# Kernel optimization log

Measured on AMD Instinct MI355X. Metric: run time of the kernel, lower is better.

## Reference

```python
import jax, jax.numpy as jnp
import numpy as np

B, S, H = 8, 2048, 1024
G, K = 16, 320          # n_groups, codebook_size
D = H // G              # codebook_dim per group


def setup_inputs() -> dict:
    key = jax.random.key(0)
    k1, k2, k3, k4 = jax.random.split(key, 4)
    inputs = jax.random.normal(k1, (B, S, H), jnp.float32)
    attention_mask = jax.random.uniform(k2, (B, S)) < 0.9
    W_cb = jax.random.normal(k3, (D, K), jnp.float32) * 0.05  # shared codebook projection
    b_cb = jnp.zeros((K,), jnp.float32)
    codevectors = jax.random.normal(k4, (K, D), jnp.float32) * 0.05
    return {"inputs": inputs, "attention_mask": attention_mask,
            "W_cb": W_cb, "b_cb": b_cb, "codevectors": codevectors}


def reference(inputs, attention_mask, W_cb, b_cb, codevectors):
    # inputs: [B,S,H]; split H into G groups of D (tensor_split, dim=-1)
    Bs, Ss, Hs = inputs.shape
    Ks, Ds = codevectors.shape
    Gs = Hs // Ds
    x = inputs.reshape(Bs, Ss, Gs, Ds)                              # [B,S,G,D]
    logits = jnp.einsum('bsgd,dk->bsgk', x, W_cb) + b_cb            # grouped codebook logits
    # training path, gumbel_softmax=False: probs = log_softmax(logits).exp() = softmax
    probs = jax.nn.softmax(logits, axis=-1)                         # [B,S,G,K]
    cv = jnp.einsum('bsgk,kd->bsgd', probs, codevectors)            # choice(probs, codevectors)
    cv = cv.reshape(Bs, Ss, Hs)
    # scatter back into zero-padded tensors: positions outside the mask stay zero
    cv = jnp.where(attention_mask[:, :, None], cv, 0.0)             # [B,S,H]
    codewords = jnp.argmax(logits, axis=-1)                         # [B,S,G]
    codewords = jnp.where(attention_mask[:, :, None], codewords, 0)
    return cv, codewords
```

## Files before the change

### kernel.cpp

```cpp
#include <hip/hip_runtime.h>
#include <math.h>

typedef _Float16 f16;
typedef _Float16 f16x2 __attribute__((ext_vector_type(2)));
typedef _Float16 f16x8 __attribute__((ext_vector_type(8)));
typedef short short8 __attribute__((ext_vector_type(8)));
typedef float f32x4 __attribute__((ext_vector_type(4)));

#define NROWS (8 * 2048 * 16)
#define BLOCK 512
#define WAVES 8
#define NITER 8
#define GRID 256
#define TAU2 4.4e-4f
#define LOG2E 1.4426950408889634f
#define MEXP 6.0f
#define EXP2F(x) __builtin_amdgcn_exp2f(x)

__device__ __forceinline__ short f2bf(float f) {
    unsigned u = __builtin_bit_cast(unsigned, f);
    return (short)((u + 0x7fffu + ((u >> 16) & 1u)) >> 16);
}
__device__ __forceinline__ float bf2f(short h) {
    return __builtin_bit_cast(float, ((unsigned)(unsigned short)h) << 16);
}
__device__ __forceinline__ f16x2 pkrtz(float a, float b) {
    return __builtin_bit_cast(f16x2, __builtin_amdgcn_cvt_pkrtz(a, b));
}

template <int HB>
__device__ __forceinline__ void half_pass(
    const short* __restrict__ Wh, const short* __restrict__ Wl,
    const f16* __restrict__ CVp, const float* __restrict__ bs,
    const short8 (&xh)[2], const short8 (&xl)[2],
    int l15, int lg, int wb0, int wb1, int bsb, int cvb,
    f32x4 (&cv)[4], float& sum_run,
    float& m1o, float& m2o, int& i1o, int& c0, int& c1, int& c2)
{
    f32x4 acc[10];
    __builtin_amdgcn_s_setprio(1);
    #pragma unroll
    for (int nt = 0; nt < 10; ++nt) {
        const int ntg = HB / 16 + nt;
        acc[nt] = *(const f32x4*)&bs[ntg * 16 + bsb];
        short8 whf0 = *(const short8*)&Wh[ntg * 1024 + wb0];
        short8 wlf0 = *(const short8*)&Wl[ntg * 1024 + wb0];
        acc[nt] = __builtin_amdgcn_mfma_f32_16x16x32_bf16(whf0, xl[0], acc[nt], 0, 0, 0);
        acc[nt] = __builtin_amdgcn_mfma_f32_16x16x32_bf16(wlf0, xh[0], acc[nt], 0, 0, 0);
        acc[nt] = __builtin_amdgcn_mfma_f32_16x16x32_bf16(whf0, xh[0], acc[nt], 0, 0, 0);
        short8 whf1 = *(const short8*)&Wh[ntg * 1024 + wb1];
        short8 wlf1 = *(const short8*)&Wl[ntg * 1024 + wb1];
        acc[nt] = __builtin_amdgcn_mfma_f32_16x16x32_bf16(whf1, xl[1], acc[nt], 0, 0, 0);
        acc[nt] = __builtin_amdgcn_mfma_f32_16x16x32_bf16(wlf1, xh[1], acc[nt], 0, 0, 0);
        acc[nt] = __builtin_amdgcn_mfma_f32_16x16x32_bf16(whf1, xh[1], acc[nt], 0, 0, 0);
    }
    __builtin_amdgcn_s_setprio(0);

    float m1a = -INFINITY, m2a = -INFINITY, m1b = -INFINITY, m2b = -INFINITY;
    int i1a = HB, i1b = HB + 80;
    #pragma unroll
    for (int nt = 0; nt < 5; ++nt) {
        #pragma unroll
        for (int r = 0; r < 4; ++r) {
            float va = acc[nt][r];
            m2a = fmaxf(m2a, fminf(m1a, va));
            if (va > m1a) { m1a = va; i1a = HB + nt * 16 + lg * 4 + r; }
            float vb = acc[nt + 5][r];
            m2b = fmaxf(m2b, fminf(m1b, vb));
            if (vb > m1b) { m1b = vb; i1b = HB + (nt + 5) * 16 + lg * 4 + r; }
        }
    }

    float sA = 0.f, sB = 0.f, sC = 0.f, sD = 0.f;
    #pragma unroll
    for (int lp = 0; lp < 5; ++lp) {
        const int pg = HB / 32 + lp;
        float q0 = EXP2F(acc[lp * 2][0] - MEXP);
        float q1 = EXP2F(acc[lp * 2][1] - MEXP);
        float q2 = EXP2F(acc[lp * 2][2] - MEXP);
        float q3 = EXP2F(acc[lp * 2][3] - MEXP);
        float q4 = EXP2F(acc[lp * 2 + 1][0] - MEXP);
        float q5 = EXP2F(acc[lp * 2 + 1][1] - MEXP);
        float q6 = EXP2F(acc[lp * 2 + 1][2] - MEXP);
        float q7 = EXP2F(acc[lp * 2 + 1][3] - MEXP);
        sA += q0 + q4; sB += q1 + q5; sC += q2 + q6; sD += q3 + q7;
        f16x2 a01 = pkrtz(q0, q1), a23 = pkrtz(q2, q3);
        f16x2 a45 = pkrtz(q4, q5), a67 = pkrtz(q6, q7);
        f16x8 pf = {a01[0], a01[1], a23[0], a23[1],
                    a45[0], a45[1], a67[0], a67[1]};
        #pragma unroll
        for (int dt = 0; dt < 4; ++dt) {
            f16x8 cf = *(const f16x8*)&CVp[(pg * 4 + dt) * 512 + cvb];
            cv[dt] = __builtin_amdgcn_mfma_f32_16x16x32_f16(cf, pf, cv[dt], 0, 0, 0);
        }
    }
    sum_run += (sA + sB) + (sC + sD);

    float m2 = fmaxf(fmaxf(m2a, m2b), fminf(m1a, m1b));
    float m1 = m1a;
    int i1 = i1a;
    if (m1b > m1) { m1 = m1b; i1 = i1b; }
    #pragma unroll
    for (int dx = 16; dx <= 32; dx <<= 1) {
        float mo = __shfl_xor(m1, dx, 64);
        int io = __shfl_xor(i1, dx, 64);
        float m2x = __shfl_xor(m2, dx, 64);
        m2 = fmaxf(fmaxf(m2, m2x), fminf(m1, mo));
        if (mo > m1 || (mo == m1 && io < i1)) { m1 = mo; i1 = io; }
    }

    c0 = -1; c1 = -1; c2 = -1;
    if (m1 - m2 < TAU2) {
        const float thr = m1 - TAU2;
        #pragma unroll
        for (int nt = 0; nt < 10; ++nt) {
            #pragma unroll
            for (int r = 0; r < 4; ++r) {
                if (acc[nt][r] >= thr) {
                    int c = HB + nt * 16 + lg * 4 + r;
                    if (c0 < 0) c0 = c;
                    else if (c1 < 0) c1 = c;
                    else if (c2 < 0) c2 = c;
                }
            }
        }
    }
    m1o = m1; m2o = m2; i1o = i1;
}

__global__ __launch_bounds__(BLOCK) void vq_mfma(
    const float* __restrict__ inputs,
    const int* __restrict__ mask,
    const float* __restrict__ Wcb,
    const float* __restrict__ bcb,
    const float* __restrict__ codevec,
    float* __restrict__ out_cv,
    float* __restrict__ out_cw)
{
    __shared__ __align__(16) short Wh[320 * 64];
    __shared__ __align__(16) short Wl[320 * 64];
    __shared__ __align__(16) f16 CVp[20480];
    __shared__ __align__(16) float bs[320];

    const int tid = threadIdx.x;

    for (int e = tid; e < 64 * 320; e += BLOCK) {
        int d = e / 320, n = e - d * 320;
        float w = Wcb[e] * LOG2E;
        short wh = f2bf(w);
        short wl = f2bf(w - bf2f(wh));
        int s = d >> 3;
        int idx = n * 64 + (((s ^ n) & 7) << 3) + (d & 7);
        Wh[idx] = wh;
        Wl[idx] = wl;
    }
    for (int e = tid; e < 320 * 64; e += BLOCK) {
        int c = e >> 6, d = e & 63;
        int p = c >> 5, tp = (c >> 4) & 1, tc = c & 15;
        int lgc = tc >> 2, r = tc & 3;
        int ee = (tp << 2) | r;
        int dt = d >> 4, m = d & 15;
        CVp[(p * 4 + dt) * 512 + m * 32 + (((lgc ^ (m >> 1)) & 3) << 3) + ee] =
            (f16)codevec[e];
    }
    for (int e = tid; e < 320; e += BLOCK) bs[e] = bcb[e] * LOG2E;
    __syncthreads();

    const int wid = tid >> 6;
    const int lane = tid & 63;
    const int l15 = lane & 15;
    const int lg = lane >> 4;
    const int l7 = l15 & 7;
    const int u = blockIdx.x * WAVES + wid;

    const int wb0 = l15 * 64 + (((lg ^ l7) & 7) << 3);
    const int wb1 = l15 * 64 + ((((4 + lg) ^ l7) & 7) << 3);
    const int bsb = lg * 4;
    const int cvb = l15 * 32 + (((lg ^ (l15 >> 1)) & 3) << 3);

    #pragma unroll 1
    for (int it = 0; it < NITER; ++it) {
        const int row0 = u * (NITER * 16) + it * 16;
        const float* xrow = inputs + (size_t)(row0 + l15) * 64;

        short8 xh[2], xl[2];
        #pragma unroll
        for (int kc = 0; kc < 2; ++kc) {
            float4 a = *(const float4*)(xrow + kc * 32 + lg * 8);
            float4 b = *(const float4*)(xrow + kc * 32 + lg * 8 + 4);
            float xv[8] = {a.x, a.y, a.z, a.w, b.x, b.y, b.z, b.w};
            short8 h, l;
            #pragma unroll
            for (int e = 0; e < 8; ++e) {
                short hh = f2bf(xv[e]);
                h[e] = hh;
                l[e] = f2bf(xv[e] - bf2f(hh));
            }
            xh[kc] = h;
            xl[kc] = l;
        }

        f32x4 cv[4];
        #pragma unroll
        for (int dt = 0; dt < 4; ++dt) cv[dt] = (f32x4){0.f, 0.f, 0.f, 0.f};
        float sum_run = 0.f;
        float m1A, m2A, m1B, m2B;
        int i1A, i1B, cA0, cA1, cA2, cB0, cB1, cB2;

        half_pass<0>(Wh, Wl, CVp, bs, xh, xl, l15, lg,
                     wb0, wb1, bsb, cvb,
                     cv, sum_run, m1A, m2A, i1A, cA0, cA1, cA2);
        half_pass<160>(Wh, Wl, CVp, bs, xh, xl, l15, lg,
                       wb0, wb1, bsb, cvb,
                       cv, sum_run, m1B, m2B, i1B, cB0, cB1, cB2);

        float m1 = m1A;
        int i1 = i1A;
        float m2 = fmaxf(fmaxf(m2A, m2B), fminf(m1A, m1B));
        if (m1B > m1) { m1 = m1B; i1 = i1B; }

        float sum = sum_run;
        sum += __shfl_xor(sum, 16, 64);
        sum += __shfl_xor(sum, 32, 64);

        const int mk = mask[u * NITER + it];
        int cw = i1;
        const bool flag = mk && (m1 - m2 < TAU2);
        if (__any(flag)) {
            float bv = -INFINITY;
            int bi = 0x7fffffff;
            #pragma unroll 1
            for (int t = 0; t < 8; ++t) {
                int c = (t == 0) ? i1A : (t == 1) ? i1B :
                        (t == 2) ? cA0 : (t == 3) ? cA1 : (t == 4) ? cA2 :
                        (t == 5) ? cB0 : (t == 6) ? cB1 : cB2;
                if (!flag) c = -1;
                if (__any(c >= 0)) {
                    if (c >= 0) {
                        float sacc = bcb[c];
                        #pragma unroll 4
                        for (int q = 0; q < 16; ++q) {
                            float4 xv4 = *(const float4*)(xrow + q * 4);
                            sacc = fmaf(xv4.x, Wcb[(q * 4 + 0) * 320 + c], sacc);
                            sacc = fmaf(xv4.y, Wcb[(q * 4 + 1) * 320 + c], sacc);
                            sacc = fmaf(xv4.z, Wcb[(q * 4 + 2) * 320 + c], sacc);
                            sacc = fmaf(xv4.w, Wcb[(q * 4 + 3) * 320 + c], sacc);
                        }
                        if (sacc > bv || (sacc == bv && c < bi)) { bv = sacc; bi = c; }
                    }
                }
            }
            #pragma unroll
            for (int dx = 16; dx <= 32; dx <<= 1) {
                float vo = __shfl_xor(bv, dx, 64);
                int io = __shfl_xor(bi, dx, 64);
                if (vo > bv || (vo == bv && io < bi)) { bv = vo; bi = io; }
            }
            if (flag) cw = bi;
        }

        const float inv = mk ? (1.0f / sum) : 0.0f;
        float* orow = out_cv + (size_t)(row0 + l15) * 64;
        #pragma unroll
        for (int dt = 0; dt < 4; ++dt) {
            f32x4 v;
            v[0] = cv[dt][0] * inv;
            v[1] = cv[dt][1] * inv;
            v[2] = cv[dt][2] * inv;
            v[3] = cv[dt][3] * inv;
            *(f32x4*)(orow + dt * 16 + lg * 4) = v;
        }
        if (lg == 0) out_cw[row0 + l15] = mk ? (float)cw : 0.0f;
    }
}

extern "C" void kernel_launch(void* const* d_in, const int* in_sizes, int n_in,
                              void* d_out, int out_size, void* d_ws, size_t ws_size,
                              hipStream_t stream) {
    const float* inputs  = (const float*)d_in[0];
    const int*   mask    = (const int*)d_in[1];
    const float* Wcb     = (const float*)d_in[2];
    const float* bcb     = (const float*)d_in[3];
    const float* codevec = (const float*)d_in[4];

    float* out_cv = (float*)d_out;
    float* out_cw = out_cv + (size_t)NROWS * 64;

    vq_mfma<<<GRID, BLOCK, 0, stream>>>(inputs, mask, Wcb, bcb, codevec,
                                        out_cv, out_cw);
}
```

Before: 84.03 us.

## Prefetch next input tile into LDS via async global_load_lds

Each wave now stages its 16-row input tile into a private LDS buffer using global_load_lds, with a swizzled layout, and issues the load for the next iteration right after the current tile has been read into registers. This overlaps global memory latency with the MFMA/softmax work of the current iteration instead of stalling on direct global loads. It adds 32KB of LDS per block, which may lower occupancy, and relies on explicit waitcnt/sched barriers for correctness.

```diff
diff --git a/kernel.cpp b/kernel.cpp
--- a/kernel.cpp
+++ b/kernel.cpp
@@ -26,6 +26,11 @@
 }
 __device__ __forceinline__ f16x2 pkrtz(float a, float b) {
     return __builtin_bit_cast(f16x2, __builtin_amdgcn_cvt_pkrtz(a, b));
+}
+__device__ __forceinline__ void gload_lds16(const void* g, void* l) {
+    __builtin_amdgcn_global_load_lds(
+        (const __attribute__((address_space(1))) unsigned int*)g,
+        (__attribute__((address_space(3))) unsigned int*)l, 16, 0, 0);
 }
 
 template <int HB>
@@ -141,6 +146,7 @@
     __shared__ __align__(16) short Wl[320 * 64];
     __shared__ __align__(16) f16 CVp[20480];
     __shared__ __align__(16) float bs[320];
+    __shared__ __align__(16) float xs[WAVES][1024];
 
     const int tid = threadIdx.x;
 
@@ -178,16 +184,37 @@
     const int bsb = lg * 4;
     const int cvb = l15 * 32 + (((lg ^ (l15 >> 1)) & 3) << 3);
 
+    char* xsw = (char*)&xs[wid][0];
+    int goff[4];
+    #pragma unroll
+    for (int i = 0; i < 4; ++i) {
+        int o = i * 1024 + lane * 16;
+        int r = o >> 8;
+        int ch = ((o >> 4) & 15) ^ (r & 7);
+        goff[i] = r * 256 + ch * 16;
+    }
+
+    {
+        const char* src = (const char*)(inputs + (size_t)u * (NITER * 16) * 64);
+        #pragma unroll
+        for (int i = 0; i < 4; ++i)
+            gload_lds16(src + goff[i], xsw + i * 1024);
+    }
+
     #pragma unroll 1
     for (int it = 0; it < NITER; ++it) {
         const int row0 = u * (NITER * 16) + it * 16;
         const float* xrow = inputs + (size_t)(row0 + l15) * 64;
 
+        asm volatile("s_waitcnt vmcnt(0)" ::: "memory");
+        __builtin_amdgcn_sched_barrier(0);
         short8 xh[2], xl[2];
         #pragma unroll
         for (int kc = 0; kc < 2; ++kc) {
-            float4 a = *(const float4*)(xrow + kc * 32 + lg * 8);
-            float4 b = *(const float4*)(xrow + kc * 32 + lg * 8 + 4);
+            int ca = (kc * 8 + lg * 2) ^ l7;
+            int cb = (kc * 8 + lg * 2 + 1) ^ l7;
+            float4 a = *(const float4*)&xs[wid][l15 * 64 + (ca << 2)];
+            float4 b = *(const float4*)&xs[wid][l15 * 64 + (cb << 2)];
             float xv[8] = {a.x, a.y, a.z, a.w, b.x, b.y, b.z, b.w};
             short8 h, l;
             #pragma unroll
@@ -198,6 +225,15 @@
             }
             xh[kc] = h;
             xl[kc] = l;
+        }
+        asm volatile("s_waitcnt lgkmcnt(0)" ::: "memory");
+        __builtin_amdgcn_sched_barrier(0);
+        if (it + 1 < NITER) {
+            const char* src = (const char*)(inputs +
+                (size_t)(u * (NITER * 16) + (it + 1) * 16) * 64);
+            #pragma unroll
+            for (int i = 0; i < 4; ++i)
+                gload_lds16(src + goff[i], xsw + i * 1024);
         }
 
         f32x4 cv[4];
```

After: 92.21 us. 1.1x slower.
